# Kernel optimization log

Measured on AMD Instinct MI355X. Metric: run time of the kernel, lower is better.

Reference implementation:

```python
import jax, jax.numpy as jnp
import numpy as np

N = 100000   # nodes
E = 1600000  # edges (avg degree 16)
D = 128      # input feature dim
H = 128      # hidden_channels
O = 64       # out_channels


def _uniform(key, shape, fan_in):
    bound = 1.0 / np.sqrt(fan_in)
    return jax.random.uniform(key, shape, jnp.float32, -bound, bound)


def setup_inputs() -> dict:
    key = jax.random.key(0)
    ks = jax.random.split(key, 9)
    x = jax.random.normal(ks[0], (N, D), jnp.float32)
    edge_index = jax.random.randint(ks[1], (2, E), 0, N, dtype=jnp.int32)
    return {
        "x": x,
        "edge_index": edge_index,
        # layer 1: SAGEConv(D -> H): lin_l (on aggregated neighbors, with bias), lin_r (root)
        "W1l": _uniform(ks[2], (D, H), D),
        "b1": _uniform(ks[3], (H,), D),
        "W1r": _uniform(ks[4], (D, H), D),
        # layer 2: SAGEConv(H -> O)
        "W2l": _uniform(ks[5], (H, O), H),
        "b2": _uniform(ks[6], (O,), H),
        "W2r": _uniform(ks[7], (H, O), H),
    }


def sage_conv(x, edge_index, Wl, b, Wr):
    """PyG SAGEConv with mean aggregation: lin_l(mean_{j in N(i)} x_j) + lin_r(x_i)."""
    src, dst = edge_index[0], edge_index[1]
    n = x.shape[0]
    msg = x[src]                                                 # [E, D] gather
    agg = jax.ops.segment_sum(msg, dst, num_segments=n)         # [N, D] scatter-add
    cnt = jax.ops.segment_sum(jnp.ones((src.shape[0],), x.dtype), dst, num_segments=n)
    agg = agg / jnp.maximum(cnt, 1.0)[:, None]                  # mean; isolated nodes -> 0
    return agg @ Wl + b + x @ Wr


def reference(x, edge_index, W1l, b1, W1r, W2l, b2, W2r):
    h = jax.nn.relu(sage_conv(x, edge_index, W1l, b1, W1r))
    return sage_conv(h, edge_index, W2l, b2, W2r)
```

## Files before the change

### kernel.cpp

```cpp
#include <hip/hip_runtime.h>
#include <stdint.h>

#define NN 100000
#define NE 1600000
#define MAXDEG 64
#define NSLICE 8
#define SLICE_SZ 12500
#define CHUNK 6400

typedef __attribute__((ext_vector_type(8))) short short8;
typedef __attribute__((ext_vector_type(4))) float f32x4;

__device__ __forceinline__ float bflo(unsigned v) { return __uint_as_float(v << 16); }
__device__ __forceinline__ float bfhi(unsigned v) { return __uint_as_float(v & 0xffff0000u); }
__device__ __forceinline__ unsigned short f2bf(float f) {
  unsigned u = __float_as_uint(f);
  u += 0x7fff + ((u >> 16) & 1);
  return (unsigned short)(u >> 16);
}

__global__ __launch_bounds__(256) void build_buckets(const int* __restrict__ src,
                                                     const int* __restrict__ dst,
                                                     int* __restrict__ cnt,
                                                     int* __restrict__ buck) {
  const int slice = blockIdx.x & (NSLICE - 1);
  const int chunk = blockIdx.x >> 3;
  const int c0 = chunk * CHUNK;
  const int lo = slice * SLICE_SZ, hi = lo + SLICE_SZ;
  for (int e = c0 + (int)threadIdx.x * 4; e < c0 + CHUNK; e += 1024) {
    int4 d = *(const int4*)(dst + e);
    int4 s = *(const int4*)(src + e);
    if (d.x >= lo && d.x < hi) { int p = atomicAdd(&cnt[d.x], 1); if (p < MAXDEG) buck[d.x * MAXDEG + p] = s.x; }
    if (d.y >= lo && d.y < hi) { int p = atomicAdd(&cnt[d.y], 1); if (p < MAXDEG) buck[d.y * MAXDEG + p] = s.y; }
    if (d.z >= lo && d.z < hi) { int p = atomicAdd(&cnt[d.z], 1); if (p < MAXDEG) buck[d.z * MAXDEG + p] = s.z; }
    if (d.w >= lo && d.w < hi) { int p = atomicAdd(&cnt[d.w], 1); if (p < MAXDEG) buck[d.w * MAXDEG + p] = s.w; }
  }
}

__global__ __launch_bounds__(256) void to_bf16(const float* __restrict__ x,
                                               unsigned* __restrict__ xb) {
  int i = blockIdx.x * 256 + threadIdx.x;
  if (i >= NN * 32) return;
  float4 v = ((const float4*)x)[i];
  uint2 o;
  o.x = ((unsigned)f2bf(v.y) << 16) | f2bf(v.x);
  o.y = ((unsigned)f2bf(v.w) << 16) | f2bf(v.z);
  ((uint2*)xb)[i] = o;
}

__global__ __launch_bounds__(256) void transpose_w(const float* __restrict__ W1l,
                                                   const float* __restrict__ W1r,
                                                   const float* __restrict__ W2l,
                                                   const float* __restrict__ W2r,
                                                   unsigned short* __restrict__ WT1,
                                                   unsigned short* __restrict__ WT2p) {
  int t = blockIdx.x * 256 + threadIdx.x;
  if (t < 128 * 256) {
    int m = t >> 8, k = t & 255;
    float v = (k < 128) ? W1l[k * 128 + m] : W1r[(k - 128) * 128 + m];
    WT1[t] = f2bf(v);
  } else {
    int i = t - 128 * 256;
    if (i < 128 * 128) {
      int m = i >> 7, k = i & 127;
      float v = (m < 64) ? W2l[k * 64 + m] : W2r[k * 64 + (m - 64)];
      WT2p[i] = f2bf(v);
    }
  }
}

template <int M, bool RELU, typename OutT>
__global__ __launch_bounds__(256) void sage_fused(const unsigned* __restrict__ xb,
                                                  const int* __restrict__ cnt,
                                                  const int* __restrict__ buck,
                                                  const unsigned short* __restrict__ WT,
                                                  const float* __restrict__ bias,
                                                  OutT* __restrict__ out) {
  constexpr int LDA = 264;
  __shared__ unsigned short sA[64][LDA];

  const int t = threadIdx.x;
  const int lane = t & 63;
  const int wv = t >> 6;
  const int node0 = blockIdx.x * 64;
  const int nb = node0 + wv * 16;

  int slot[16]; unsigned xr[16]; int deg[16];
#pragma unroll
  for (int i = 0; i < 16; i++) {
    int node = nb + i;
    if (node < NN) {
      slot[i] = buck[(size_t)node * MAXDEG + lane];
      xr[i]   = xb[(size_t)node * 64 + lane];
      deg[i]  = cnt[node];
    } else { slot[i] = 0; xr[i] = 0u; deg[i] = 0; }
  }

#pragma unroll
  for (int i = 0; i < 16; i++) {
    float a0 = 0.f, a1 = 0.f;
    int dcl = min(deg[i], MAXDEG);
    if (dcl > 0) {
      int last = dcl - 1;
      for (int p = 0; p < dcl; p += 16) {
        unsigned v[16];
#pragma unroll
        for (int j = 0; j < 16; j++) {
          int s = __shfl(slot[i], min(p + j, last), 64);
          v[j] = xb[(size_t)s * 64 + lane];
        }
#pragma unroll
        for (int j = 0; j < 16; j++) {
          unsigned vj = (p + j <= last) ? v[j] : 0u;
          a0 += bflo(vj); a1 += bfhi(vj);
        }
      }
    }
    float inv = 1.f / (float)max(deg[i], 1);
    unsigned pk = ((unsigned)f2bf(a1 * inv) << 16) | f2bf(a0 * inv);
    ((unsigned*)&sA[wv * 16 + i][0])[lane]   = pk;
    ((unsigned*)&sA[wv * 16 + i][128])[lane] = xr[i];
  }

  const int m = lane & 15;
  const int q = lane >> 4;

  f32x4 acc[M / 16];
#pragma unroll
  for (int c = 0; c < M / 16; c++) acc[c] = {0.f, 0.f, 0.f, 0.f};

#pragma unroll
  for (int ks = 0; ks < 8; ks++) {
    short8 a = *(const short8*)&sA[wv * 16 + m][ks * 32 + q * 8];
#pragma unroll
    for (int c = 0; c < M / 16; c++) {
      short8 b = *(const short8*)(WT + (size_t)(c * 16 + m) * 256 + ks * 32 + q * 8);
      acc[c] = __builtin_amdgcn_mfma_f32_16x16x32_bf16(a, b, acc[c], 0, 0, 0);
    }
  }

#pragma unroll
  for (int c = 0; c < M / 16; c++) {
    int col = c * 16 + m;
    float bc = bias[col];
#pragma unroll
    for (int r = 0; r < 4; r++) {
      int lr = wv * 16 + q * 4 + r;
      float v = acc[c][r] + bc;
      if (RELU) v = fmaxf(v, 0.f);
      if constexpr (sizeof(OutT) == 2) sA[lr][col] = f2bf(v);
      else ((float*)&sA[lr][0])[col] = v;
    }
  }
#pragma unroll
  for (int it = 0; it < 4; it++) {
    int idx = it * 64 + lane;
    int rr = idx >> 4, cc = idx & 15;
    int node = node0 + wv * 16 + rr;
    if (node < NN) {
      uint4 v = *(const uint4*)((const char*)&sA[wv * 16 + rr][0] + cc * 16);
      *(uint4*)((char*)(out + (size_t)node * M) + cc * 16) = v;
    }
  }
}

__global__ __launch_bounds__(256) void proj2(const unsigned* __restrict__ hb,
                                             const unsigned short* __restrict__ WTp,
                                             const float* __restrict__ b2,
                                             unsigned* __restrict__ p,
                                             float* __restrict__ out) {
  __shared__ unsigned short sA[64][136];
  const int lane = threadIdx.x & 63, wv = threadIdx.x >> 6;
  const int node0 = blockIdx.x * 64, nb = node0 + wv * 16;

#pragma unroll
  for (int i = 0; i < 16; i++) {
    int node = nb + i;
    unsigned v = (node < NN) ? hb[(size_t)node * 64 + lane] : 0u;
    ((unsigned*)&sA[wv * 16 + i][0])[lane] = v;
  }

  const int m = lane & 15, q = lane >> 4;
  f32x4 acc[8];
#pragma unroll
  for (int cc = 0; cc < 8; cc++) acc[cc] = {0.f, 0.f, 0.f, 0.f};
#pragma unroll
  for (int ks = 0; ks < 4; ks++) {
    short8 a = *(const short8*)&sA[wv * 16 + m][ks * 32 + q * 8];
#pragma unroll
    for (int cc = 0; cc < 8; cc++) {
      short8 b = *(const short8*)(WTp + (size_t)(cc * 16 + m) * 128 + ks * 32 + q * 8);
      acc[cc] = __builtin_amdgcn_mfma_f32_16x16x32_bf16(a, b, acc[cc], 0, 0, 0);
    }
  }

#pragma unroll
  for (int cc = 0; cc < 4; cc++) {
    int col = cc * 16 + m;
#pragma unroll
    for (int r = 0; r < 4; r++) {
      int lr = wv * 16 + q * 4 + r;
      sA[lr][col] = f2bf(acc[cc][r]);
    }
  }
#pragma unroll
  for (int it = 0; it < 2; it++) {
    int idx = it * 64 + lane;
    int rr = idx >> 3, ck = idx & 7;
    int node = nb + rr;
    if (node < NN) {
      uint4 v = *(const uint4*)((const char*)&sA[wv * 16 + rr][0] + ck * 16);
      *(uint4*)((char*)(p + (size_t)node * 32) + ck * 16) = v;
    }
  }
#pragma unroll
  for (int cc = 4; cc < 8; cc++) {
    int col = (cc - 4) * 16 + m;
    float bc = b2[col];
#pragma unroll
    for (int r = 0; r < 4; r++) {
      int lr = wv * 16 + q * 4 + r;
      ((float*)&sA[lr][0])[col] = acc[cc][r] + bc;
    }
  }
#pragma unroll
  for (int it = 0; it < 4; it++) {
    int idx = it * 64 + lane;
    int rr = idx >> 4, ck = idx & 15;
    int node = nb + rr;
    if (node < NN) {
      uint4 v = *(const uint4*)((const char*)&sA[wv * 16 + rr][0] + ck * 16);
      *(uint4*)((char*)(out + (size_t)node * 64) + ck * 16) = v;
    }
  }
}

__global__ __launch_bounds__(256) void gather_add(const unsigned* __restrict__ p,
                                                  const int* __restrict__ cnt,
                                                  const int* __restrict__ buck,
                                                  float* __restrict__ out) {
  const int lane = threadIdx.x & 63, wv = threadIdx.x >> 6;
  const int nb = blockIdx.x * 64 + wv * 16;
  const int g = lane >> 5, c = lane & 31;

  int slot[16]; int deg[16];
#pragma unroll
  for (int i = 0; i < 16; i++) {
    int node = nb + i;
    if (node < NN) {
      slot[i] = buck[(size_t)node * MAXDEG + lane];
      deg[i]  = cnt[node];
    } else { slot[i] = 0; deg[i] = 0; }
  }

#pragma unroll
  for (int i = 0; i < 16; i++) {
    float a0 = 0.f, a1 = 0.f;
    int d = min(deg[i], MAXDEG);
    if (d > 0) {
      int last = d - 1;
      for (int pp = 0; pp < d; pp += 16) {
        unsigned v[8];
#pragma unroll
        for (int j = 0; j < 8; j++) {
          int e = pp + 2 * j + g;
          int s = __shfl(slot[i], e < last ? e : last, 64);
          v[j] = p[(size_t)s * 32 + c];
        }
#pragma unroll
        for (int j = 0; j < 8; j++) {
          int e = pp + 2 * j + g;
          unsigned w = (e <= last) ? v[j] : 0u;
          a0 += bflo(w); a1 += bfhi(w);
        }
      }
      a0 += __shfl_xor(a0, 32, 64);
      a1 += __shfl_xor(a1, 32, 64);
    }
    int node = nb + i;
    if (node < NN && lane < 32) {
      float inv = 1.f / (float)max(deg[i], 1);
      float2* fp = (float2*)(out + (size_t)node * 64 + 2 * c);
      float2 tv = *fp;
      tv.x += a0 * inv; tv.y += a1 * inv;
      *fp = tv;
    }
  }
}

extern "C" void kernel_launch(void* const* d_in, const int* in_sizes, int n_in,
                              void* d_out, int out_size, void* d_ws, size_t ws_size,
                              hipStream_t stream) {
  const float* x   = (const float*)d_in[0];
  const int*   ei  = (const int*)d_in[1];
  const float* W1l = (const float*)d_in[2];
  const float* b1  = (const float*)d_in[3];
  const float* W1r = (const float*)d_in[4];
  const float* W2l = (const float*)d_in[5];
  const float* b2  = (const float*)d_in[6];
  const float* W2r = (const float*)d_in[7];
  float* out = (float*)d_out;

  char* ws = (char*)d_ws;
  int* cnt  = (int*)ws;                                   ws += (512 << 10);
  int* buck = (int*)ws;                                   ws += (size_t)NN * MAXDEG * 4;
  unsigned* xbf = (unsigned*)ws;                          ws += (size_t)NN * 64 * 4;
  unsigned* hb = (unsigned*)ws;                           ws += (size_t)NN * 64 * 4;
  unsigned short* WT1 = (unsigned short*)ws;              ws += 128 * 256 * 2;
  unsigned short* WT2p = (unsigned short*)ws;             ws += 128 * 128 * 2;
  unsigned* ptab = xbf;

  const int* src = ei;
  const int* dst = ei + NE;

  hipMemsetAsync(cnt, 0, (size_t)NN * 4, stream);
  build_buckets<<<NSLICE * (NE / CHUNK), 256, 0, stream>>>(src, dst, cnt, buck);
  to_bf16<<<(NN * 32 + 255) / 256, 256, 0, stream>>>(x, xbf);
  transpose_w<<<192, 256, 0, stream>>>(W1l, W1r, W2l, W2r, WT1, WT2p);

  sage_fused<128, true, unsigned short><<<(NN + 63) / 64, 256, 0, stream>>>(
      xbf, cnt, buck, WT1, b1, (unsigned short*)hb);

  proj2<<<(NN + 63) / 64, 256, 0, stream>>>(hb, WT2p, b2, ptab, out);

  gather_add<<<(NN + 63) / 64, 256, 0, stream>>>(ptab, cnt, buck, out);
}
```

Before: 388.0 us.

## Project before aggregating in layer 1 and split gathers across XCD halves

Layer 1 is reordered: a new proj1 kernel applies both weight matrices first, then gather1 averages the projected neighbour rows and adds the root term with ReLU. Both gather kernels now remap block IDs so each group of four XCDs handles only half the feature columns. This shrinks the per-XCD gathered working set so it fits better in L2 and cuts random-access traffic to HBM. The cost is an extra full-size bf16 intermediate write and read, and buffers reused in place (px over xbf, h over rh), which depends on each block touching only its own rows.

```diff
diff --git a/kernel.cpp b/kernel.cpp
--- a/kernel.cpp
+++ b/kernel.cpp
@@ -7,6 +7,8 @@
 #define NSLICE 8
 #define SLICE_SZ 12500
 #define CHUNK 6400
+#define NBLK 1563
+#define GGRID 3128
 
 typedef __attribute__((ext_vector_type(8))) short short8;
 typedef __attribute__((ext_vector_type(4))) float f32x4;
@@ -52,224 +54,132 @@
                                                    const float* __restrict__ W1r,
                                                    const float* __restrict__ W2l,
                                                    const float* __restrict__ W2r,
-                                                   unsigned short* __restrict__ WT1,
-                                                   unsigned short* __restrict__ WT2p) {
+                                                   unsigned short* __restrict__ WT1P,
+                                                   unsigned short* __restrict__ WT2P) {
   int t = blockIdx.x * 256 + threadIdx.x;
-  if (t < 128 * 256) {
-    int m = t >> 8, k = t & 255;
-    float v = (k < 128) ? W1l[k * 128 + m] : W1r[(k - 128) * 128 + m];
-    WT1[t] = f2bf(v);
+  if (t < 256 * 128) {
+    int m = t >> 7, k = t & 127;
+    float v = (m < 128) ? W1l[k * 128 + m] : W1r[k * 128 + (m - 128)];
+    WT1P[t] = f2bf(v);
   } else {
-    int i = t - 128 * 256;
+    int i = t - 256 * 128;
     if (i < 128 * 128) {
       int m = i >> 7, k = i & 127;
       float v = (m < 64) ? W2l[k * 64 + m] : W2r[k * 64 + (m - 64)];
-      WT2p[i] = f2bf(v);
-    }
-  }
-}
-
-template <int M, bool RELU, typename OutT>
-__global__ __launch_bounds__(256) void sage_fused(const unsigned* __restrict__ xb,
-                                                  const int* __restrict__ cnt,
-                                                  const int* __restrict__ buck,
-                                                  const unsigned short* __restrict__ WT,
-                                                  const float* __restrict__ bias,
-                                                  OutT* __restrict__ out) {
-  constexpr int LDA = 264;
-  __shared__ unsigned short sA[64][LDA];
-
-  const int t = threadIdx.x;
-  const int lane = t & 63;
-  const int wv = t >> 6;
-  const int node0 = blockIdx.x * 64;
-  const int nb = node0 + wv * 16;
-
-  int slot[16]; unsigned xr[16]; int deg[16];
-#pragma unroll
-  for (int i = 0; i < 16; i++) {
-    int node = nb + i;
-    if (node < NN) {
-      slot[i] = buck[(size_t)node * MAXDEG + lane];
-      xr[i]   = xb[(size_t)node * 64 + lane];
-      deg[i]  = cnt[node];
-    } else { slot[i] = 0; xr[i] = 0u; deg[i] = 0; }
-  }
-
-#pragma unroll
-  for (int i = 0; i < 16; i++) {
-    float a0 = 0.f, a1 = 0.f;
-    int dcl = min(deg[i], MAXDEG);
-    if (dcl > 0) {
-      int last = dcl - 1;
-      for (int p = 0; p < dcl; p += 16) {
-        unsigned v[16];
-#pragma unroll
-        for (int j = 0; j < 16; j++) {
-          int s = __shfl(slot[i], min(p + j, last), 64);
-          v[j] = xb[(size_t)s * 64 + lane];
-        }
-#pragma unroll
-        for (int j = 0; j < 16; j++) {
-          unsigned vj = (p + j <= last) ? v[j] : 0u;
-          a0 += bflo(vj); a1 += bfhi(vj);
-        }
-      }
-    }
-    float inv = 1.f / (float)max(deg[i], 1);
-    unsigned pk = ((unsigned)f2bf(a1 * inv) << 16) | f2bf(a0 * inv);
-    ((unsigned*)&sA[wv * 16 + i][0])[lane]   = pk;
-    ((unsigned*)&sA[wv * 16 + i][128])[lane] = xr[i];
-  }
-
-  const int m = lane & 15;
-  const int q = lane >> 4;
-
-  f32x4 acc[M / 16];
-#pragma unroll
-  for (int c = 0; c < M / 16; c++) acc[c] = {0.f, 0.f, 0.f, 0.f};
-
-#pragma unroll
-  for (int ks = 0; ks < 8; ks++) {
+      WT2P[i] = f2bf(v);
+    }
+  }
+}
+
+__global__ __launch_bounds__(256) void proj1(const unsigned* __restrict__ xb,
+                                             const unsigned short* __restrict__ WTP,
+                                             const float* __restrict__ b1,
+                                             unsigned short* __restrict__ px,
+                                             unsigned short* __restrict__ r) {
+  __shared__ unsigned short sA[64][264];
+  const int lane = threadIdx.x & 63, wv = threadIdx.x >> 6;
+  const int nb = blockIdx.x * 64 + wv * 16;
+
+#pragma unroll
+  for (int i = 0; i < 16; i++) {
+    int node = nb + i;
+    unsigned v = (node < NN) ? xb[(size_t)node * 64 + lane] : 0u;
+    ((unsigned*)&sA[wv * 16 + i][0])[lane] = v;
+  }
+
+  const int m = lane & 15, q = lane >> 4;
+  f32x4 acc[16];
+#pragma unroll
+  for (int cc = 0; cc < 16; cc++) acc[cc] = {0.f, 0.f, 0.f, 0.f};
+#pragma unroll
+  for (int ks = 0; ks < 4; ks++) {
     short8 a = *(const short8*)&sA[wv * 16 + m][ks * 32 + q * 8];
 #pragma unroll
-    for (int c = 0; c < M / 16; c++) {
-      short8 b = *(const short8*)(WT + (size_t)(c * 16 + m) * 256 + ks * 32 + q * 8);
-      acc[c] = __builtin_amdgcn_mfma_f32_16x16x32_bf16(a, b, acc[c], 0, 0, 0);
-    }
-  }
-
-#pragma unroll
-  for (int c = 0; c < M / 16; c++) {
-    int col = c * 16 + m;
-    float bc = bias[col];
-#pragma unroll
-    for (int r = 0; r < 4; r++) {
-      int lr = wv * 16 + q * 4 + r;
-      float v = acc[c][r] + bc;
-      if (RELU) v = fmaxf(v, 0.f);
-      if constexpr (sizeof(OutT) == 2) sA[lr][col] = f2bf(v);
-      else ((float*)&sA[lr][0])[col] = v;
+    for (int cc = 0; cc < 16; cc++) {
+      short8 b = *(const short8*)(WTP + (size_t)(cc * 16 + m) * 128 + ks * 32 + q * 8);
+      acc[cc] = __builtin_amdgcn_mfma_f32_16x16x32_bf16(a, b, acc[cc], 0, 0, 0);
+    }
+  }
+
+#pragma unroll
+  for (int cc = 0; cc < 16; cc++) {
+    int col = cc * 16 + m;
+    float bc = (col >= 128) ? b1[col - 128] : 0.f;
+#pragma unroll
+    for (int rr = 0; rr < 4; rr++) {
+      int lr = wv * 16 + q * 4 + rr;
+      sA[lr][col] = f2bf(acc[cc][rr] + bc);
     }
   }
 #pragma unroll
   for (int it = 0; it < 4; it++) {
     int idx = it * 64 + lane;
-    int rr = idx >> 4, cc = idx & 15;
-    int node = node0 + wv * 16 + rr;
-    if (node < NN) {
-      uint4 v = *(const uint4*)((const char*)&sA[wv * 16 + rr][0] + cc * 16);
-      *(uint4*)((char*)(out + (size_t)node * M) + cc * 16) = v;
-    }
-  }
-}
-
-__global__ __launch_bounds__(256) void proj2(const unsigned* __restrict__ hb,
-                                             const unsigned short* __restrict__ WTp,
-                                             const float* __restrict__ b2,
-                                             unsigned* __restrict__ p,
-                                             float* __restrict__ out) {
-  __shared__ unsigned short sA[64][136];
-  const int lane = threadIdx.x & 63, wv = threadIdx.x >> 6;
-  const int node0 = blockIdx.x * 64, nb = node0 + wv * 16;
-
-#pragma unroll
-  for (int i = 0; i < 16; i++) {
-    int node = nb + i;
-    unsigned v = (node < NN) ? hb[(size_t)node * 64 + lane] : 0u;
-    ((unsigned*)&sA[wv * 16 + i][0])[lane] = v;
-  }
-
-  const int m = lane & 15, q = lane >> 4;
-  f32x4 acc[8];
-#pragma unroll
-  for (int cc = 0; cc < 8; cc++) acc[cc] = {0.f, 0.f, 0.f, 0.f};
-#pragma unroll
-  for (int ks = 0; ks < 4; ks++) {
-    short8 a = *(const short8*)&sA[wv * 16 + m][ks * 32 + q * 8];
-#pragma unroll
-    for (int cc = 0; cc < 8; cc++) {
-      short8 b = *(const short8*)(WTp + (size_t)(cc * 16 + m) * 128 + ks * 32 + q * 8);
-      acc[cc] = __builtin_amdgcn_mfma_f32_16x16x32_bf16(a, b, acc[cc], 0, 0, 0);
-    }
-  }
-
-#pragma unroll
-  for (int cc = 0; cc < 4; cc++) {
-    int col = cc * 16 + m;
-#pragma unroll
-    for (int r = 0; r < 4; r++) {
-      int lr = wv * 16 + q * 4 + r;
-      sA[lr][col] = f2bf(acc[cc][r]);
-    }
-  }
-#pragma unroll
-  for (int it = 0; it < 2; it++) {
-    int idx = it * 64 + lane;
-    int rr = idx >> 3, ck = idx & 7;
-    int node = nb + rr;
-    if (node < NN) {
-      uint4 v = *(const uint4*)((const char*)&sA[wv * 16 + rr][0] + ck * 16);
-      *(uint4*)((char*)(p + (size_t)node * 32) + ck * 16) = v;
-    }
-  }
-#pragma unroll
-  for (int cc = 4; cc < 8; cc++) {
-    int col = (cc - 4) * 16 + m;
-    float bc = b2[col];
-#pragma unroll
-    for (int r = 0; r < 4; r++) {
-      int lr = wv * 16 + q * 4 + r;
-      ((float*)&sA[lr][0])[col] = acc[cc][r] + bc;
+    int rrow = idx >> 4, ck = idx & 15;
+    int node = nb + rrow;
+    if (node < NN) {
+      uint4 v = *(const uint4*)((const char*)&sA[wv * 16 + rrow][0] + ck * 16);
+      *(uint4*)((char*)(px + (size_t)node * 128) + ck * 16) = v;
     }
   }
 #pragma unroll
   for (int it = 0; it < 4; it++) {
     int idx = it * 64 + lane;
-    int rr = idx >> 4, ck = idx & 15;
-    int node = nb + rr;
-    if (node < NN) {
-      uint4 v = *(const uint4*)((const char*)&sA[wv * 16 + rr][0] + ck * 16);
-      *(uint4*)((char*)(out + (size_t)node * 64) + ck * 16) = v;
-    }
-  }
-}
-
-__global__ __launch_bounds__(256) void gather_add(const unsigned* __restrict__ p,
-                                                  const int* __restrict__ cnt,
-                                                  const int* __restrict__ buck,
-                                                  float* __restrict__ out) {
+    int rrow = idx >> 4, ck = idx & 15;
+    int node = nb + rrow;
+    if (node < NN) {
+      uint4 v = *(const uint4*)((const char*)&sA[wv * 16 + rrow][0] + 256 + ck * 16);
+      *(uint4*)((char*)(r + (size_t)node * 128) + ck * 16) = v;
+    }
+  }
+}
+
+__global__ __launch_bounds__(256) void gather1(const unsigned short* __restrict__ px,
+                                               const unsigned short* __restrict__ rt,
+                                               const int* __restrict__ cnt,
+                                               const int* __restrict__ buck,
+                                               unsigned short* __restrict__ h) {
+  const int b = blockIdx.x;
+  const int xcd = b & 7;
+  const int half = xcd >> 2;
+  const int nbi = (b >> 3) * 4 + (xcd & 3);
+  if (nbi >= NBLK) return;
   const int lane = threadIdx.x & 63, wv = threadIdx.x >> 6;
-  const int nb = blockIdx.x * 64 + wv * 16;
+  const int nb = nbi * 64 + wv * 16;
   const int g = lane >> 5, c = lane & 31;
-
-  int slot[16]; int deg[16];
-#pragma unroll
-  for (int i = 0; i < 16; i++) {
-    int node = nb + i;
-    if (node < NN) {
-      slot[i] = buck[(size_t)node * MAXDEG + lane];
+  const unsigned* pxw = (const unsigned*)px;
+
+  int slot[16]; int deg[16]; unsigned rr[16];
+#pragma unroll
+  for (int i = 0; i < 16; i++) {
+    int node = nb + i;
+    if (node < NN) {
+      slot[i] = buck[(size_t)node * MAXDEG + (lane & 31)];
       deg[i]  = cnt[node];
-    } else { slot[i] = 0; deg[i] = 0; }
+      rr[i]   = ((const unsigned*)rt)[(size_t)node * 64 + half * 32 + c];
+    } else { slot[i] = 0; deg[i] = 0; rr[i] = 0u; }
   }
 
 #pragma unroll
   for (int i = 0; i < 16; i++) {
     float a0 = 0.f, a1 = 0.f;
+    int node = nb + i;
     int d = min(deg[i], MAXDEG);
+    if (d > 32) {
+      if (lane >= 32) slot[i] = buck[(size_t)node * MAXDEG + lane];
+    }
     if (d > 0) {
       int last = d - 1;
-      for (int pp = 0; pp < d; pp += 16) {
+      for (int p = 0; p < d; p += 16) {
         unsigned v[8];
 #pragma unroll
         for (int j = 0; j < 8; j++) {
-          int e = pp + 2 * j + g;
+          int e = p + 2 * j + g;
           int s = __shfl(slot[i], e < last ? e : last, 64);
-          v[j] = p[(size_t)s * 32 + c];
+          v[j] = pxw[(size_t)s * 64 + half * 32 + c];
         }
 #pragma unroll
         for (int j = 0; j < 8; j++) {
-          int e = pp + 2 * j + g;
+          int e = p + 2 * j + g;
           unsigned w = (e <= last) ? v[j] : 0u;
           a0 += bflo(w); a1 += bfhi(w);
         }
@@ -277,10 +187,144 @@
       a0 += __shfl_xor(a0, 32, 64);
       a1 += __shfl_xor(a1, 32, 64);
     }
-    int node = nb + i;
     if (node < NN && lane < 32) {
       float inv = 1.f / (float)max(deg[i], 1);
-      float2* fp = (float2*)(out + (size_t)node * 64 + 2 * c);
+      float h0 = fmaxf(a0 * inv + bflo(rr[i]), 0.f);
+      float h1 = fmaxf(a1 * inv + bfhi(rr[i]), 0.f);
+      ((unsigned*)h)[(size_t)node * 64 + half * 32 + c] =
+          ((unsigned)f2bf(h1) << 16) | f2bf(h0);
+    }
+  }
+}
+
+__global__ __launch_bounds__(256) void proj2(const unsigned* __restrict__ hb,
+                                             const unsigned short* __restrict__ WTP,
+                                             const float* __restrict__ b2,
+                                             unsigned short* __restrict__ p2,
+                                             float* __restrict__ out) {
+  __shared__ unsigned short sA[64][136];
+  const int lane = threadIdx.x & 63, wv = threadIdx.x >> 6;
+  const int nb = blockIdx.x * 64 + wv * 16;
+
+#pragma unroll
+  for (int i = 0; i < 16; i++) {
+    int node = nb + i;
+    unsigned v = (node < NN) ? hb[(size_t)node * 64 + lane] : 0u;
+    ((unsigned*)&sA[wv * 16 + i][0])[lane] = v;
+  }
+
+  const int m = lane & 15, q = lane >> 4;
+  f32x4 acc[8];
+#pragma unroll
+  for (int cc = 0; cc < 8; cc++) acc[cc] = {0.f, 0.f, 0.f, 0.f};
+#pragma unroll
+  for (int ks = 0; ks < 4; ks++) {
+    short8 a = *(const short8*)&sA[wv * 16 + m][ks * 32 + q * 8];
+#pragma unroll
+    for (int cc = 0; cc < 8; cc++) {
+      short8 b = *(const short8*)(WTP + (size_t)(cc * 16 + m) * 128 + ks * 32 + q * 8);
+      acc[cc] = __builtin_amdgcn_mfma_f32_16x16x32_bf16(a, b, acc[cc], 0, 0, 0);
+    }
+  }
+
+#pragma unroll
+  for (int cc = 0; cc < 4; cc++) {
+    int col = cc * 16 + m;
+#pragma unroll
+    for (int rr = 0; rr < 4; rr++) {
+      int lr = wv * 16 + q * 4 + rr;
+      sA[lr][col] = f2bf(acc[cc][rr]);
+    }
+  }
+  {
+    int rrow = lane >> 2, ck = lane & 3;
+    int node = nb + rrow;
+    if (node < NN) {
+      uint4 vlo = *(const uint4*)((const char*)&sA[wv * 16 + rrow][0] + ck * 16);
+      *(uint4*)((char*)(p2 + (size_t)node * 32) + ck * 16) = vlo;
+      uint4 vhi = *(const uint4*)((const char*)&sA[wv * 16 + rrow][0] + 64 + ck * 16);
+      *(uint4*)((char*)(p2 + (size_t)NN * 32 + (size_t)node * 32) + ck * 16) = vhi;
+    }
+  }
+#pragma unroll
+  for (int cc = 4; cc < 8; cc++) {
+    int col = (cc - 4) * 16 + m;
+    float bc = b2[col];
+#pragma unroll
+    for (int rr = 0; rr < 4; rr++) {
+      int lr = wv * 16 + q * 4 + rr;
+      ((float*)&sA[lr][0])[col] = acc[cc][rr] + bc;
+    }
+  }
+#pragma unroll
+  for (int it = 0; it < 4; it++) {
+    int idx = it * 64 + lane;
+    int rrow = idx >> 4, ck = idx & 15;
+    int node = nb + rrow;
+    if (node < NN) {
+      uint4 v = *(const uint4*)((const char*)&sA[wv * 16 + rrow][0] + ck * 16);
+      *(uint4*)((char*)(out + (size_t)node * 64) + ck * 16) = v;
+    }
+  }
+}
+
+__global__ __launch_bounds__(256) void gather2(const unsigned short* __restrict__ p2,
+                                               const int* __restrict__ cnt,
+                                               const int* __restrict__ buck,
+                                               float* __restrict__ out) {
+  const int b = blockIdx.x;
+  const int xcd = b & 7;
+  const int half = xcd >> 2;
+  const int nbi = (b >> 3) * 4 + (xcd & 3);
+  if (nbi >= NBLK) return;
+  const int lane = threadIdx.x & 63, wv = threadIdx.x >> 6;
+  const int nb = nbi * 64 + wv * 16;
+  const int sub = lane >> 4, cl = lane & 15;
+  const unsigned* pw = (const unsigned*)(p2 + (size_t)half * NN * 32);
+
+  int slot[16]; int deg[16];
+#pragma unroll
+  for (int i = 0; i < 16; i++) {
+    int node = nb + i;
+    if (node < NN) {
+      slot[i] = buck[(size_t)node * MAXDEG + (lane & 31)];
+      deg[i]  = cnt[node];
+    } else { slot[i] = 0; deg[i] = 0; }
+  }
+
+#pragma unroll
+  for (int i = 0; i < 16; i++) {
+    float a0 = 0.f, a1 = 0.f;
+    int node = nb + i;
+    int d = min(deg[i], MAXDEG);
+    if (d > 32) {
+      if (lane >= 32) slot[i] = buck[(size_t)node * MAXDEG + lane];
+    }
+    if (d > 0) {
+      int last = d - 1;
+      for (int p = 0; p < d; p += 16) {
+        unsigned v[4];
+#pragma unroll
+        for (int j = 0; j < 4; j++) {
+          int e = p + 4 * j + sub;
+          int s = __shfl(slot[i], e < last ? e : last, 64);
+          v[j] = pw[(size_t)s * 16 + cl];
+        }
+#pragma unroll
+        for (int j = 0; j < 4; j++) {
+          int e = p + 4 * j + sub;
+          unsigned w = (e <= last) ? v[j] : 0u;
+          a0 += bflo(w); a1 += bfhi(w);
+        }
+      }
+      a0 += __shfl_xor(a0, 16, 64);
+      a0 += __shfl_xor(a0, 32, 64);
+      a1 += __shfl_xor(a1, 16, 64);
+      a1 += __shfl_xor(a1, 32, 64);
+    }
+    if (node < NN && lane < 16) {
+      float inv = 1.f / (float)max(deg[i], 1);
+      float2* fp = (float2*)(out + (size_t)node * 64 + half * 32 + cl * 2);
       float2 tv = *fp;
       tv.x += a0 * inv; tv.y += a1 * inv;
       *fp = tv;
@@ -305,10 +349,11 @@
   int* cnt  = (int*)ws;                                   ws += (512 << 10);
   int* buck = (int*)ws;                                   ws += (size_t)NN * MAXDEG * 4;
   unsigned* xbf = (unsigned*)ws;                          ws += (size_t)NN * 64 * 4;
-  unsigned* hb = (unsigned*)ws;                           ws += (size_t)NN * 64 * 4;
-  unsigned short* WT1 = (unsigned short*)ws;              ws += 128 * 256 * 2;
-  unsigned short* WT2p = (unsigned short*)ws;             ws += 128 * 128 * 2;
-  unsigned* ptab = xbf;
+  unsigned short* rh = (unsigned short*)ws;               ws += (size_t)NN * 128 * 2;
+  unsigned short* WT1P = (unsigned short*)ws;             ws += 256 * 128 * 2;
+  unsigned short* WT2P = (unsigned short*)ws;             ws += 128 * 128 * 2;
+  unsigned short* px = (unsigned short*)xbf;
+  unsigned short* p2 = (unsigned short*)xbf;
 
   const int* src = ei;
   const int* dst = ei + NE;
@@ -316,12 +361,11 @@
   hipMemsetAsync(cnt, 0, (size_t)NN * 4, stream);
   build_buckets<<<NSLICE * (NE / CHUNK), 256, 0, stream>>>(src, dst, cnt, buck);
   to_bf16<<<(NN * 32 + 255) / 256, 256, 0, stream>>>(x, xbf);
-  transpose_w<<<192, 256, 0, stream>>>(W1l, W1r, W2l, W2r, WT1, WT2p);
-
-  sage_fused<128, true, unsigned short><<<(NN + 63) / 64, 256, 0, stream>>>(
-      xbf, cnt, buck, WT1, b1, (unsigned short*)hb);
-
-  proj2<<<(NN + 63) / 64, 256, 0, stream>>>(hb, WT2p, b2, ptab, out);
-
-  gather_add<<<(NN + 63) / 64, 256, 0, stream>>>(ptab, cnt, buck, out);
-}
+  transpose_w<<<192, 256, 0, stream>>>(W1l, W1r, W2l, W2r, WT1P, WT2P);
+
+  proj1<<<NBLK, 256, 0, stream>>>(xbf, WT1P, b1, px, rh);
+  gather1<<<GGRID, 256, 0, stream>>>(px, rh, cnt, buck, rh);
+
+  proj2<<<NBLK, 256, 0, stream>>>((const unsigned*)rh, WT2P, b2, p2, out);
+  gather2<<<GGRID, 256, 0, stream>>>(p2, cnt, buck, out);
+}
```

After: 467.7 us. 1.21x slower.

## Fuse prep kernels and split layer-2 gather into XCD-mapped column halves

Applied to the files above, without the earlier changes.

Merges bucket building, bf16 conversion and weight transpose into a single prep launch to cut launch overhead. Layer-2 projection output is stored as two separate column-half tables, and the gather kernel launches twice as many blocks, each handling one half. Blocks are mapped so each group of four XCDs reads only one half-table, aiming at better L2 locality on the random neighbor gathers. The cost is more blocks, each repeating the bucket and count reads, plus narrower 64-byte row fetches.

```diff
diff --git a/kernel.cpp b/kernel.cpp
--- a/kernel.cpp
+++ b/kernel.cpp
@@ -7,6 +7,13 @@
 #define NSLICE 8
 #define SLICE_SZ 12500
 #define CHUNK 6400
+#define NBLK 1563
+#define GGRID 3128
+
+#define BB_BLOCKS 2000
+#define TB_BLOCKS 12500
+#define TW_BLOCKS 192
+#define PREP_BLOCKS (BB_BLOCKS + TB_BLOCKS + TW_BLOCKS)
 
 typedef __attribute__((ext_vector_type(8))) short short8;
 typedef __attribute__((ext_vector_type(4))) float f32x4;
@@ -19,52 +26,52 @@
   return (unsigned short)(u >> 16);
 }
 
-__global__ __launch_bounds__(256) void build_buckets(const int* __restrict__ src,
-                                                     const int* __restrict__ dst,
-                                                     int* __restrict__ cnt,
-                                                     int* __restrict__ buck) {
-  const int slice = blockIdx.x & (NSLICE - 1);
-  const int chunk = blockIdx.x >> 3;
-  const int c0 = chunk * CHUNK;
-  const int lo = slice * SLICE_SZ, hi = lo + SLICE_SZ;
-  for (int e = c0 + (int)threadIdx.x * 4; e < c0 + CHUNK; e += 1024) {
-    int4 d = *(const int4*)(dst + e);
-    int4 s = *(const int4*)(src + e);
-    if (d.x >= lo && d.x < hi) { int p = atomicAdd(&cnt[d.x], 1); if (p < MAXDEG) buck[d.x * MAXDEG + p] = s.x; }
-    if (d.y >= lo && d.y < hi) { int p = atomicAdd(&cnt[d.y], 1); if (p < MAXDEG) buck[d.y * MAXDEG + p] = s.y; }
-    if (d.z >= lo && d.z < hi) { int p = atomicAdd(&cnt[d.z], 1); if (p < MAXDEG) buck[d.z * MAXDEG + p] = s.z; }
-    if (d.w >= lo && d.w < hi) { int p = atomicAdd(&cnt[d.w], 1); if (p < MAXDEG) buck[d.w * MAXDEG + p] = s.w; }
-  }
-}
-
-__global__ __launch_bounds__(256) void to_bf16(const float* __restrict__ x,
-                                               unsigned* __restrict__ xb) {
-  int i = blockIdx.x * 256 + threadIdx.x;
-  if (i >= NN * 32) return;
-  float4 v = ((const float4*)x)[i];
-  uint2 o;
-  o.x = ((unsigned)f2bf(v.y) << 16) | f2bf(v.x);
-  o.y = ((unsigned)f2bf(v.w) << 16) | f2bf(v.z);
-  ((uint2*)xb)[i] = o;
-}
-
-__global__ __launch_bounds__(256) void transpose_w(const float* __restrict__ W1l,
-                                                   const float* __restrict__ W1r,
-                                                   const float* __restrict__ W2l,
-                                                   const float* __restrict__ W2r,
-                                                   unsigned short* __restrict__ WT1,
-                                                   unsigned short* __restrict__ WT2p) {
-  int t = blockIdx.x * 256 + threadIdx.x;
-  if (t < 128 * 256) {
-    int m = t >> 8, k = t & 255;
-    float v = (k < 128) ? W1l[k * 128 + m] : W1r[(k - 128) * 128 + m];
-    WT1[t] = f2bf(v);
+__global__ __launch_bounds__(256) void prep(const int* __restrict__ src,
+                                            const int* __restrict__ dst,
+                                            int* __restrict__ cnt,
+                                            int* __restrict__ buck,
+                                            const float* __restrict__ x,
+                                            unsigned* __restrict__ xb,
+                                            const float* __restrict__ W1l,
+                                            const float* __restrict__ W1r,
+                                            const float* __restrict__ W2l,
+                                            const float* __restrict__ W2r,
+                                            unsigned short* __restrict__ WT1,
+                                            unsigned short* __restrict__ WT2p) {
+  const int b = blockIdx.x;
+  if (b < BB_BLOCKS) {
+    const int slice = b & (NSLICE - 1);
+    const int chunk = b >> 3;
+    const int c0 = chunk * CHUNK;
+    const int lo = slice * SLICE_SZ, hi = lo + SLICE_SZ;
+    for (int e = c0 + (int)threadIdx.x * 4; e < c0 + CHUNK; e += 1024) {
+      int4 d = *(const int4*)(dst + e);
+      int4 s = *(const int4*)(src + e);
+      if (d.x >= lo && d.x < hi) { int p = atomicAdd(&cnt[d.x], 1); if (p < MAXDEG) buck[d.x * MAXDEG + p] = s.x; }
+      if (d.y >= lo && d.y < hi) { int p = atomicAdd(&cnt[d.y], 1); if (p < MAXDEG) buck[d.y * MAXDEG + p] = s.y; }
+      if (d.z >= lo && d.z < hi) { int p = atomicAdd(&cnt[d.z], 1); if (p < MAXDEG) buck[d.z * MAXDEG + p] = s.z; }
+      if (d.w >= lo && d.w < hi) { int p = atomicAdd(&cnt[d.w], 1); if (p < MAXDEG) buck[d.w * MAXDEG + p] = s.w; }
+    }
+  } else if (b < BB_BLOCKS + TB_BLOCKS) {
+    int i = (b - BB_BLOCKS) * 256 + threadIdx.x;
+    float4 v = ((const float4*)x)[i];
+    uint2 o;
+    o.x = ((unsigned)f2bf(v.y) << 16) | f2bf(v.x);
+    o.y = ((unsigned)f2bf(v.w) << 16) | f2bf(v.z);
+    ((uint2*)xb)[i] = o;
   } else {
-    int i = t - 128 * 256;
-    if (i < 128 * 128) {
-      int m = i >> 7, k = i & 127;
-      float v = (m < 64) ? W2l[k * 64 + m] : W2r[k * 64 + (m - 64)];
-      WT2p[i] = f2bf(v);
+    int t = (b - BB_BLOCKS - TB_BLOCKS) * 256 + threadIdx.x;
+    if (t < 128 * 256) {
+      int m = t >> 8, k = t & 255;
+      float v = (k < 128) ? W1l[k * 128 + m] : W1r[(k - 128) * 128 + m];
+      WT1[t] = f2bf(v);
+    } else {
+      int i = t - 128 * 256;
+      if (i < 128 * 128) {
+        int m = i >> 7, k = i & 127;
+        float v = (m < 64) ? W2l[k * 64 + m] : W2r[k * 64 + (m - 64)];
+        WT2p[i] = f2bf(v);
+      }
     }
   }
 }
@@ -165,13 +172,13 @@
 }
 
 __global__ __launch_bounds__(256) void proj2(const unsigned* __restrict__ hb,
-                                             const unsigned short* __restrict__ WTp,
+                                             const unsigned short* __restrict__ WTP,
                                              const float* __restrict__ b2,
-                                             unsigned* __restrict__ p,
+                                             unsigned short* __restrict__ p2,
                                              float* __restrict__ out) {
   __shared__ unsigned short sA[64][136];
   const int lane = threadIdx.x & 63, wv = threadIdx.x >> 6;
-  const int node0 = blockIdx.x * 64, nb = node0 + wv * 16;
+  const int nb = blockIdx.x * 64 + wv * 16;
 
 #pragma unroll
   for (int i = 0; i < 16; i++) {
@@ -189,7 +196,7 @@
     short8 a = *(const short8*)&sA[wv * 16 + m][ks * 32 + q * 8];
 #pragma unroll
     for (int cc = 0; cc < 8; cc++) {
-      short8 b = *(const short8*)(WTp + (size_t)(cc * 16 + m) * 128 + ks * 32 + q * 8);
+      short8 b = *(const short8*)(WTP + (size_t)(cc * 16 + m) * 128 + ks * 32 + q * 8);
       acc[cc] = __builtin_amdgcn_mfma_f32_16x16x32_bf16(a, b, acc[cc], 0, 0, 0);
     }
   }
@@ -198,19 +205,19 @@
   for (int cc = 0; cc < 4; cc++) {
     int col = cc * 16 + m;
 #pragma unroll
-    for (int r = 0; r < 4; r++) {
-      int lr = wv * 16 + q * 4 + r;
-      sA[lr][col] = f2bf(acc[cc][r]);
-    }
-  }
-#pragma unroll
-  for (int it = 0; it < 2; it++) {
-    int idx = it * 64 + lane;
-    int rr = idx >> 3, ck = idx & 7;
-    int node = nb + rr;
-    if (node < NN) {
-      uint4 v = *(const uint4*)((const char*)&sA[wv * 16 + rr][0] + ck * 16);
-      *(uint4*)((char*)(p + (size_t)node * 32) + ck * 16) = v;
+    for (int rr = 0; rr < 4; rr++) {
+      int lr = wv * 16 + q * 4 + rr;
+      sA[lr][col] = f2bf(acc[cc][rr]);
+    }
+  }
+  {
+    int rrow = lane >> 2, ck = lane & 3;
+    int node = nb + rrow;
+    if (node < NN) {
+      uint4 vlo = *(const uint4*)((const char*)&sA[wv * 16 + rrow][0] + ck * 16);
+      *(uint4*)((char*)(p2 + (size_t)node * 32) + ck * 16) = vlo;
+      uint4 vhi = *(const uint4*)((const char*)&sA[wv * 16 + rrow][0] + 64 + ck * 16);
+      *(uint4*)((char*)(p2 + (size_t)NN * 32 + (size_t)node * 32) + ck * 16) = vhi;
     }
   }
 #pragma unroll
@@ -218,37 +225,43 @@
     int col = (cc - 4) * 16 + m;
     float bc = b2[col];
 #pragma unroll
-    for (int r = 0; r < 4; r++) {
-      int lr = wv * 16 + q * 4 + r;
-      ((float*)&sA[lr][0])[col] = acc[cc][r] + bc;
+    for (int rr = 0; rr < 4; rr++) {
+      int lr = wv * 16 + q * 4 + rr;
+      ((float*)&sA[lr][0])[col] = acc[cc][rr] + bc;
     }
   }
 #pragma unroll
   for (int it = 0; it < 4; it++) {
     int idx = it * 64 + lane;
-    int rr = idx >> 4, ck = idx & 15;
-    int node = nb + rr;
-    if (node < NN) {
-      uint4 v = *(const uint4*)((const char*)&sA[wv * 16 + rr][0] + ck * 16);
+    int rrow = idx >> 4, ck = idx & 15;
+    int node = nb + rrow;
+    if (node < NN) {
+      uint4 v = *(const uint4*)((const char*)&sA[wv * 16 + rrow][0] + ck * 16);
       *(uint4*)((char*)(out + (size_t)node * 64) + ck * 16) = v;
     }
   }
 }
 
-__global__ __launch_bounds__(256) void gather_add(const unsigned* __restrict__ p,
-                                                  const int* __restrict__ cnt,
-                                                  const int* __restrict__ buck,
-                                                  float* __restrict__ out) {
+__global__ __launch_bounds__(256) void gather2(const unsigned short* __restrict__ p2,
+                                               const int* __restrict__ cnt,
+                                               const int* __restrict__ buck,
+                                               float* __restrict__ out) {
+  const int b = blockIdx.x;
+  const int xcd = b & 7;
+  const int half = xcd >> 2;
+  const int nbi = (b >> 3) * 4 + (xcd & 3);
+  if (nbi >= NBLK) return;
   const int lane = threadIdx.x & 63, wv = threadIdx.x >> 6;
-  const int nb = blockIdx.x * 64 + wv * 16;
-  const int g = lane >> 5, c = lane & 31;
+  const int nb = nbi * 64 + wv * 16;
+  const int sub = lane >> 4, cl = lane & 15;
+  const unsigned* pw = (const unsigned*)(p2 + (size_t)half * NN * 32);
 
   int slot[16]; int deg[16];
 #pragma unroll
   for (int i = 0; i < 16; i++) {
     int node = nb + i;
     if (node < NN) {
-      slot[i] = buck[(size_t)node * MAXDEG + lane];
+      slot[i] = buck[(size_t)node * MAXDEG + (lane & 31)];
       deg[i]  = cnt[node];
     } else { slot[i] = 0; deg[i] = 0; }
   }
@@ -256,31 +269,36 @@
 #pragma unroll
   for (int i = 0; i < 16; i++) {
     float a0 = 0.f, a1 = 0.f;
+    int node = nb + i;
     int d = min(deg[i], MAXDEG);
+    if (d > 32) {
+      if (lane >= 32) slot[i] = buck[(size_t)node * MAXDEG + lane];
+    }
     if (d > 0) {
       int last = d - 1;
-      for (int pp = 0; pp < d; pp += 16) {
-        unsigned v[8];
-#pragma unroll
-        for (int j = 0; j < 8; j++) {
-          int e = pp + 2 * j + g;
+      for (int p = 0; p < d; p += 16) {
+        unsigned v[4];
+#pragma unroll
+        for (int j = 0; j < 4; j++) {
+          int e = p + 4 * j + sub;
           int s = __shfl(slot[i], e < last ? e : last, 64);
-          v[j] = p[(size_t)s * 32 + c];
+          v[j] = pw[(size_t)s * 16 + cl];
         }
 #pragma unroll
-        for (int j = 0; j < 8; j++) {
-          int e = pp + 2 * j + g;
+        for (int j = 0; j < 4; j++) {
+          int e = p + 4 * j + sub;
           unsigned w = (e <= last) ? v[j] : 0u;
           a0 += bflo(w); a1 += bfhi(w);
         }
       }
+      a0 += __shfl_xor(a0, 16, 64);
       a0 += __shfl_xor(a0, 32, 64);
+      a1 += __shfl_xor(a1, 16, 64);
       a1 += __shfl_xor(a1, 32, 64);
     }
-    int node = nb + i;
-    if (node < NN && lane < 32) {
+    if (node < NN && lane < 16) {
       float inv = 1.f / (float)max(deg[i], 1);
-      float2* fp = (float2*)(out + (size_t)node * 64 + 2 * c);
+      float2* fp = (float2*)(out + (size_t)node * 64 + half * 32 + cl * 2);
       float2 tv = *fp;
       tv.x += a0 * inv; tv.y += a1 * inv;
       *fp = tv;
@@ -308,20 +326,19 @@
   unsigned* hb = (unsigned*)ws;                           ws += (size_t)NN * 64 * 4;
   unsigned short* WT1 = (unsigned short*)ws;              ws += 128 * 256 * 2;
   unsigned short* WT2p = (unsigned short*)ws;             ws += 128 * 128 * 2;
-  unsigned* ptab = xbf;
+  unsigned short* p2 = (unsigned short*)xbf;
 
   const int* src = ei;
   const int* dst = ei + NE;
 
   hipMemsetAsync(cnt, 0, (size_t)NN * 4, stream);
-  build_buckets<<<NSLICE * (NE / CHUNK), 256, 0, stream>>>(src, dst, cnt, buck);
-  to_bf16<<<(NN * 32 + 255) / 256, 256, 0, stream>>>(x, xbf);
-  transpose_w<<<192, 256, 0, stream>>>(W1l, W1r, W2l, W2r, WT1, WT2p);
-
-  sage_fused<128, true, unsigned short><<<(NN + 63) / 64, 256, 0, stream>>>(
+  prep<<<PREP_BLOCKS, 256, 0, stream>>>(src, dst, cnt, buck, x, xbf,
+                                        W1l, W1r, W2l, W2r, WT1, WT2p);
+
+  sage_fused<128, true, unsigned short><<<NBLK, 256, 0, stream>>>(
       xbf, cnt, buck, WT1, b1, (unsigned short*)hb);
 
-  proj2<<<(NN + 63) / 64, 256, 0, stream>>>(hb, WT2p, b2, ptab, out);
-
-  gather_add<<<(NN + 63) / 64, 256, 0, stream>>>(ptab, cnt, buck, out);
-}
+  proj2<<<NBLK, 256, 0, stream>>>(hb, WT2p, b2, p2, out);
+
+  gather2<<<GGRID, 256, 0, stream>>>(p2, cnt, buck, out);
+}
```

Measured after the change: 400.7 us. +3.3%, slower.
